# Kernel tuning notes

Hardware: AMD Instinct MI355X
Metric: run time of the kernel (lower is better)

## Reference

```python
import jax, jax.numpy as jnp
import numpy as np

HEAD_NUM = 16
SCALE = 1.0 / np.sqrt(HEAD_NUM)  # source divides by sqrt(head_num), not head_dim
MASK_VAL = -10000000.0


def setup_inputs() -> dict:
    key = jax.random.key(0)
    kq, kk, kv = jax.random.split(key, 3)
    shape = (2, 16, 2048, 64)  # [B, H, L, D]
    Q = jax.random.normal(kq, shape, dtype=jnp.float32)
    K = jax.random.normal(kk, shape, dtype=jnp.float32)
    V = jax.random.normal(kv, shape, dtype=jnp.float32)
    return {"Q": Q, "K": K, "V": V}


def reference(Q, K, V):
    L = Q.shape[-2]
    # [B, H, L, M] attention logits, scaled by 1/sqrt(head_num)
    logits = jnp.einsum('bhld,bhmd->bhlm', Q, K) * SCALE
    # causal mask: strictly-upper triangle gets -1e7 (additive, as in source)
    mask = jnp.triu(jnp.ones((L, L), dtype=logits.dtype), 1) * MASK_VAL
    logits = logits + mask[None, None, :, :]
    weights = jax.nn.softmax(logits, axis=-1)
    return jnp.einsum('bhlm,bhmd->bhld', weights, V)
```

## Files before the change

kernel.cpp:

```cpp
#include <hip/hip_runtime.h>
#include <hip/hip_bf16.h>

#define BM 128
#define BN 64
#define HD 64
#define LQ 2048
#define SD 72

typedef __attribute__((ext_vector_type(8))) short short8;
typedef __attribute__((ext_vector_type(16))) float f32x16;

#define QSCALE 0.360673760222241f

#define WS_HALF  ((size_t)32 * 2048 * 64)
#define WS_NEEDED (2 * WS_HALF * sizeof(unsigned short))

static __device__ __forceinline__ unsigned pk2(float a, float b) {
    union { __hip_bfloat162 h2; unsigned u; } c;
    c.h2 = __float22bfloat162_rn(make_float2(a, b));
    return c.u;
}

__global__ __launch_bounds__(256)
void prep(const float* __restrict__ Kg, const float* __restrict__ Vg,
          unsigned short* __restrict__ KF, unsigned short* __restrict__ VF) {
    __shared__ unsigned short sK2[64][72];
    __shared__ unsigned short sV2[64][72];
    const int t  = threadIdx.x;
    const int bx = blockIdx.x;
    const int bh = bx >> 5;
    const int c  = bx & 31;
    const size_t ibase = (size_t)bh * (LQ * HD) + (size_t)c * 64 * HD;
    const int r  = t >> 4;
    const int c4 = (t & 15) * 4;

#pragma unroll
    for (int p = 0; p < 4; ++p) {
        const int row = p * 16 + r;
        const float4 kv4 = *(const float4*)(Kg + ibase + (size_t)row * HD + c4);
        uint2 ku; ku.x = pk2(kv4.x, kv4.y); ku.y = pk2(kv4.z, kv4.w);
        *(uint2*)&sK2[row][c4] = ku;
        const float4 vv4 = *(const float4*)(Vg + ibase + (size_t)row * HD + c4);
        const unsigned u0 = pk2(vv4.x, vv4.y);
        const unsigned u1 = pk2(vv4.z, vv4.w);
        sV2[c4 + 0][row] = (unsigned short)(u0 & 0xffff);
        sV2[c4 + 1][row] = (unsigned short)(u0 >> 16);
        sV2[c4 + 2][row] = (unsigned short)(u1 & 0xffff);
        sV2[c4 + 3][row] = (unsigned short)(u1 >> 16);
    }
    __syncthreads();

    const int lane = t & 63;
    const int u    = t >> 6;
    const int l31  = lane & 31;
    const int hh   = lane >> 5;
#pragma unroll
    for (int e = 0; e < 2; ++e) {
        const int ch = 2 * c + e;
        const size_t ob = ((size_t)(bh * 64 + ch) * 4 + u) * 512 + lane * 8;
        *(uint4*)&KF[ob] = *(const uint4*)&sK2[e * 32 + l31][u * 16 + hh * 8];
        *(uint4*)&VF[ob] = *(const uint4*)&sV2[(u & 1) * 32 + l31][e * 32 + (u >> 1) * 16 + hh * 8];
    }
}

__global__ __launch_bounds__(256, 2)
void fa_main(const float* __restrict__ Qg,
             const unsigned short* __restrict__ KF,
             const unsigned short* __restrict__ VF,
             float* __restrict__ Og) {
    const int t    = threadIdx.x;
    const int w    = t >> 6;
    const int lane = t & 63;
    const int h    = lane >> 5;
    const int l31  = lane & 31;

    const int bx  = blockIdx.x;
    const int idx = (bx >> 5) & 7;
    const int qt  = (bx & 256) ? idx : (15 - idx);
    const int bh  = bx & 31;
    const int q0  = qt * BM;

    const size_t base = (size_t)bh * (LQ * HD);
    const unsigned short* KFh = KF + (size_t)bh * 131072 + lane * 8;
    const unsigned short* VFh = VF + (size_t)bh * 131072 + lane * 8;

    const int qrow = q0 + w * 32 + l31;
    short8 qreg[4];
    {
        const float* Qrow = Qg + base + (size_t)qrow * HD;
#pragma unroll
        for (int ks = 0; ks < 4; ++ks) {
            const float4 a = *(const float4*)(Qrow + ks * 16 + h * 8);
            const float4 b = *(const float4*)(Qrow + ks * 16 + h * 8 + 4);
            union { unsigned u[4]; short8 s8; } qu;
            qu.u[0] = pk2(a.x * QSCALE, a.y * QSCALE);
            qu.u[1] = pk2(a.z * QSCALE, a.w * QSCALE);
            qu.u[2] = pk2(b.x * QSCALE, b.y * QSCALE);
            qu.u[3] = pk2(b.z * QSCALE, b.w * QSCALE);
            qreg[ks] = qu.s8;
        }
    }

    f32x16 accO[2];
#pragma unroll
    for (int r = 0; r < 16; ++r) { accO[0][r] = 0.f; accO[1][r] = 0.f; }
    float lsum = 0.f;

    const int n_ch = (q0 >> 5) + w + 1;
    const int last = n_ch - 1;

    auto loadch = [&](short8* ak, short8* av, int ch) {
        const unsigned short* kp = KFh + (size_t)ch * 2048;
        ak[0] = *(const short8*)(kp);
        ak[1] = *(const short8*)(kp + 512);
        ak[2] = *(const short8*)(kp + 1024);
        ak[3] = *(const short8*)(kp + 1536);
        const unsigned short* vp = VFh + (size_t)ch * 2048;
        av[0] = *(const short8*)(vp);
        av[1] = *(const short8*)(vp + 512);
        av[2] = *(const short8*)(vp + 1024);
        av[3] = *(const short8*)(vp + 1536);
    };

    auto computech = [&](const short8* ak, const short8* av, int ch) {
        f32x16 accS;
#pragma unroll
        for (int r = 0; r < 16; ++r) accS[r] = 0.f;
        __builtin_amdgcn_s_setprio(1);
#pragma unroll
        for (int ks = 0; ks < 4; ++ks)
            accS = __builtin_amdgcn_mfma_f32_32x32x16_bf16(ak[ks], qreg[ks], accS, 0, 0, 0);
        __builtin_amdgcn_s_setprio(0);

        if (ch == last) {
            const int kvb = ch * 32 + 4 * h;
#pragma unroll
            for (int r = 0; r < 16; ++r) {
                const int kv = kvb + (r & 3) + 8 * (r >> 2);
                if (kv > qrow) accS[r] = -1e30f;
            }
        }

#pragma unroll
        for (int r = 0; r < 16; ++r) {
            const float p = __builtin_amdgcn_exp2f(accS[r]);
            accS[r] = p;
            lsum += p;
        }

        short8 pf[2];
#pragma unroll
        for (int s = 0; s < 2; ++s) {
            const int rb = s * 8;
            const unsigned a0 = pk2(accS[rb + 0], accS[rb + 1]);
            const unsigned b0 = pk2(accS[rb + 4], accS[rb + 5]);
            const unsigned a1 = pk2(accS[rb + 2], accS[rb + 3]);
            const unsigned b1 = pk2(accS[rb + 6], accS[rb + 7]);
            const auto r02 = __builtin_amdgcn_permlane32_swap(a0, b0, 0, 0);
            const auto r13 = __builtin_amdgcn_permlane32_swap(a1, b1, 0, 0);
            union { unsigned u[4]; short8 s8; } pu;
            pu.u[0] = r02[0]; pu.u[1] = r13[0]; pu.u[2] = r02[1]; pu.u[3] = r13[1];
            pf[s] = pu.s8;
        }

        __builtin_amdgcn_s_setprio(1);
#pragma unroll
        for (int s = 0; s < 2; ++s)
#pragma unroll
            for (int dg = 0; dg < 2; ++dg)
                accO[dg] = __builtin_amdgcn_mfma_f32_32x32x16_bf16(av[s * 2 + dg], pf[s], accO[dg], 0, 0, 0);
        __builtin_amdgcn_s_setprio(0);
    };

    short8 akA[4], avA[4], akB[4], avB[4];
    loadch(akA, avA, 0);
    int ch = 0;
    for (;;) {
        if (ch < last) loadch(akB, avB, ch + 1);
        computech(akA, avA, ch);
        if (++ch > last) break;
        if (ch < last) loadch(akA, avA, ch + 1);
        computech(akB, avB, ch);
        if (++ch > last) break;
    }

    lsum += __shfl_xor(lsum, 32);
    const float inv = 1.0f / lsum;
    float* Op = Og + base + (size_t)qrow * HD;
#pragma unroll
    for (int dg = 0; dg < 2; ++dg) {
#pragma unroll
        for (int rq = 0; rq < 4; ++rq) {
            const int d = dg * 32 + 8 * rq + 4 * h;
            float4 o;
            o.x = accO[dg][rq * 4 + 0] * inv;
            o.y = accO[dg][rq * 4 + 1] * inv;
            o.z = accO[dg][rq * 4 + 2] * inv;
            o.w = accO[dg][rq * 4 + 3] * inv;
            *(float4*)(Op + d) = o;
        }
    }
}

__global__ __launch_bounds__(512, 4)
void fa_fwd(const float* __restrict__ Qg,
            const float* __restrict__ Kg,
            const float* __restrict__ Vg,
            float* __restrict__ Og) {
    __shared__ __align__(16) unsigned short lds[(2 * BN + 2 * HD) * SD];
    typedef unsigned short KT[BN][SD];
    typedef unsigned short VT[HD][SD];
    KT* sK  = (KT*)lds;
    VT* sVt = (VT*)(lds + 2 * BN * SD);

    const int t    = threadIdx.x;
    const int w    = t >> 6;
    const int lane = t & 63;
    const int h    = lane >> 5;
    const int l31  = lane & 31;
    const int qd   = lane >> 4;
    const int qg   = w & 3;
    const int kh   = w >> 2;

    const int bx  = blockIdx.x;
    const int idx = (bx >> 5) & 7;
    const int qt  = (bx & 256) ? idx : (15 - idx);
    const int bh  = bx & 31;
    const int q0  = qt * BM;

    const size_t base = (size_t)bh * (LQ * HD);
    const float* Qp = Qg + base + (size_t)q0 * HD;
    const float* Kp = Kg + base;
    const float* Vp = Vg + base;

    const int r0 = t >> 4;
    const int c4 = (t & 15) * 4;
    const int RA = w * 4;

    {
        unsigned short (*sQ)[SD] = (unsigned short (*)[SD])lds;
#pragma unroll
        for (int p = 0; p < 4; ++p) {
            const int r = p * 32 + r0;
            const float4 v = *(const float4*)(Qp + (size_t)r * HD + c4);
            uint2 u;
            u.x = pk2(v.x * QSCALE, v.y * QSCALE);
            u.y = pk2(v.z * QSCALE, v.w * QSCALE);
            *(uint2*)&sQ[r][c4] = u;
        }
    }
    __syncthreads();
    short8 qreg[4];
    {
        unsigned short (*sQ)[SD] = (unsigned short (*)[SD])lds;
#pragma unroll
        for (int ks = 0; ks < 4; ++ks)
            qreg[ks] = *(const short8*)&sQ[qg * 32 + l31][ks * 16 + h * 8];
    }
    __syncthreads();

    float4 kA, kB, vA, vB;
    auto issue = [&](int kv0) {
        kA = *(const float4*)(Kp + (size_t)(kv0 + r0) * HD + c4);
        kB = *(const float4*)(Kp + (size_t)(kv0 + 32 + r0) * HD + c4);
        vA = *(const float4*)(Vp + (size_t)(kv0 + RA + qd) * HD + c4);
        vB = *(const float4*)(Vp + (size_t)(kv0 + 32 + RA + qd) * HD + c4);
    };
    auto vstore = [&](float4 vf, int R, int buf) {
        float e0 = vf.x, e1 = vf.y, e2 = vf.z, e3 = vf.w;
        float s0 = (qd & 2) ? e0 : e2;
        float s1 = (qd & 2) ? e1 : e3;
        s0 = __shfl_xor(s0, 32); s1 = __shfl_xor(s1, 32);
        if (qd & 2) { e0 = s0; e1 = s1; } else { e2 = s0; e3 = s1; }
        s0 = (qd & 1) ? e0 : e1;
        s1 = (qd & 1) ? e2 : e3;
        s0 = __shfl_xor(s0, 16); s1 = __shfl_xor(s1, 16);
        if (qd & 1) { e0 = s0; e2 = s1; } else { e1 = s0; e3 = s1; }
        const int d   = c4 + qd;
        const int col = ((((R >> 3) ^ (d >> 3)) & 7) << 3) | (R & 7);
        uint2 u; u.x = pk2(e0, e1); u.y = pk2(e2, e3);
        *(uint2*)&sVt[buf][d][col] = u;
    };
    auto commit = [&](int buf) {
        { uint2 u; u.x = pk2(kA.x, kA.y); u.y = pk2(kA.z, kA.w);
          *(uint2*)&sK[buf][r0][c4] = u; }
        { uint2 u; u.x = pk2(kB.x, kB.y); u.y = pk2(kB.z, kB.w);
          *(uint2*)&sK[buf][32 + r0][c4] = u; }
        vstore(vA, RA, buf);
        vstore(vB, 32 + RA, buf);
    };

    f32x16 accO[2];
#pragma unroll
    for (int r = 0; r < 16; ++r) { accO[0][r] = 0.f; accO[1][r] = 0.f; }
    float lsum = 0.f;

    const int qminw = q0 + qg * 32;
    const int qmaxw = qminw + 31;
    const int n_it  = (q0 + BM) / BN;

    issue(0);
    commit(0);

    for (int it = 0; it < n_it; ++it) {
        const int kv0 = it * BN;
        const int buf = it & 1;
        __syncthreads();
        const bool more = (it + 1 < n_it);
        if (more) issue(kv0 + BN);

        if (kv0 + kh * 32 <= qmaxw) {
            f32x16 accS;
#pragma unroll
            for (int r = 0; r < 16; ++r) accS[r] = 0.f;
            __builtin_amdgcn_s_setprio(1);
#pragma unroll
            for (int ks = 0; ks < 4; ++ks) {
                const short8 ak = *(const short8*)&sK[buf][kh * 32 + l31][ks * 16 + h * 8];
                accS = __builtin_amdgcn_mfma_f32_32x32x16_bf16(ak, qreg[ks], accS, 0, 0, 0);
            }
            __builtin_amdgcn_s_setprio(0);

            if (kv0 + kh * 32 + 31 > qminw) {
                const int qrow = qminw + l31;
                const int kvb  = kv0 + kh * 32 + 4 * h;
#pragma unroll
                for (int r = 0; r < 16; ++r) {
                    const int kv = kvb + (r & 3) + 8 * (r >> 2);
                    if (kv > qrow) accS[r] = -1e30f;
                }
            }
#pragma unroll
            for (int r = 0; r < 16; ++r) {
                const float p = __builtin_amdgcn_exp2f(accS[r]);
                accS[r] = p;
                lsum += p;
            }
            short8 pf[2];
#pragma unroll
            for (int s = 0; s < 2; ++s) {
                const int rb = s * 8;
                const unsigned a0 = pk2(accS[rb + 0], accS[rb + 1]);
                const unsigned b0 = pk2(accS[rb + 4], accS[rb + 5]);
                const unsigned a1 = pk2(accS[rb + 2], accS[rb + 3]);
                const unsigned b1 = pk2(accS[rb + 6], accS[rb + 7]);
                const auto r02 = __builtin_amdgcn_permlane32_swap(a0, b0, 0, 0);
                const auto r13 = __builtin_amdgcn_permlane32_swap(a1, b1, 0, 0);
                union { unsigned u[4]; short8 s8; } pu;
                pu.u[0] = r02[0]; pu.u[1] = r13[0]; pu.u[2] = r02[1]; pu.u[3] = r13[1];
                pf[s] = pu.s8;
            }
            __builtin_amdgcn_s_setprio(1);
#pragma unroll
            for (int s = 0; s < 2; ++s) {
                const int K0 = kh * 32 + s * 16 + h * 8;
#pragma unroll
                for (int dg = 0; dg < 2; ++dg) {
                    const int d   = dg * 32 + l31;
                    const int col = (((K0 >> 3) ^ (d >> 3)) & 7) << 3;
                    const short8 av = *(const short8*)&sVt[buf][d][col];
                    accO[dg] = __builtin_amdgcn_mfma_f32_32x32x16_bf16(av, pf[s], accO[dg], 0, 0, 0);
                }
            }
            __builtin_amdgcn_s_setprio(0);
        }

        if (more) commit(buf ^ 1);
    }

    lsum += __shfl_xor(lsum, 32);
    __syncthreads();
    float* fx  = (float*)lds;
    float* fla = fx + 4 * 64 * 32;
    if (kh == 1) {
#pragma unroll
        for (int dg = 0; dg < 2; ++dg) {
#pragma unroll
            for (int r = 0; r < 16; ++r) {
                const int d = dg * 32 + (r & 3) + 8 * (r >> 2) + 4 * h;
                fx[(qg * 64 + d) * 32 + l31] = accO[dg][r];
            }
        }
        if (h == 0) fla[qg * 32 + l31] = lsum;
    }
    __syncthreads();
    if (kh == 0) {
        const float inv  = 1.0f / (lsum + fla[qg * 32 + l31]);
        const int   qrow = q0 + qg * 32 + l31;
        float* Op = Og + base + (size_t)qrow * HD;
#pragma unroll
        for (int dg = 0; dg < 2; ++dg) {
#pragma unroll
            for (int rq = 0; rq < 4; ++rq) {
                const int d = dg * 32 + 8 * rq + 4 * h;
                const float* fr = &fx[(qg * 64 + d) * 32 + l31];
                float4 o;
                o.x = (accO[dg][rq * 4 + 0] + fr[0])  * inv;
                o.y = (accO[dg][rq * 4 + 1] + fr[32]) * inv;
                o.z = (accO[dg][rq * 4 + 2] + fr[64]) * inv;
                o.w = (accO[dg][rq * 4 + 3] + fr[96]) * inv;
                *(float4*)(Op + d) = o;
            }
        }
    }
}

extern "C" void kernel_launch(void* const* d_in, const int* in_sizes, int n_in,
                              void* d_out, int out_size, void* d_ws, size_t ws_size,
                              hipStream_t stream) {
    const float* Q = (const float*)d_in[0];
    const float* K = (const float*)d_in[1];
    const float* V = (const float*)d_in[2];
    float* O = (float*)d_out;
    if (d_ws != nullptr && ws_size >= WS_NEEDED) {
        unsigned short* KF = (unsigned short*)d_ws;
        unsigned short* VF = KF + WS_HALF;
        prep<<<dim3(1024), dim3(256), 0, stream>>>(K, V, KF, VF);
        fa_main<<<dim3(512), dim3(256), 0, stream>>>(Q, KF, VF, O);
    } else {
        fa_fwd<<<dim3(512), dim3(512), 0, stream>>>(Q, K, V, O);
    }
}
```

Baseline: 125.0 us.

## Split KV chunks across two wave groups per query tile and reduce via LDS

fa_main now launches 512 threads per block, where two groups of four waves share each query slice and process alternating (even/odd) 32-wide KV chunks. Partial output accumulators and row sums from the odd group go through shared memory, and the even group combines them and writes the result. K is prefetched two chunks ahead while V is loaded just in time inside the compute step, which cuts register use. The aim is to double wave-level parallelism and halve the serial chunk loop per wave, at the cost of an LDS reduction, a block barrier, and higher occupancy demands.

Measured after the change: 119.0 us. 1.05x faster.

```diff
diff --git a/kernel.cpp b/kernel.cpp
--- a/kernel.cpp
+++ b/kernel.cpp
@@ -63,16 +63,21 @@
     }
 }
 
-__global__ __launch_bounds__(256, 2)
+__global__ __launch_bounds__(512, 4)
 void fa_main(const float* __restrict__ Qg,
              const unsigned short* __restrict__ KF,
              const unsigned short* __restrict__ VF,
              float* __restrict__ Og) {
+    __shared__ float fx[4 * 64 * 32];
+    __shared__ float fla[4 * 32];
+
     const int t    = threadIdx.x;
     const int w    = t >> 6;
     const int lane = t & 63;
     const int h    = lane >> 5;
     const int l31  = lane & 31;
+    const int qg   = w & 3;
+    const int kp   = w >> 2;
 
     const int bx  = blockIdx.x;
     const int idx = (bx >> 5) & 7;
@@ -84,7 +89,9 @@
     const unsigned short* KFh = KF + (size_t)bh * 131072 + lane * 8;
     const unsigned short* VFh = VF + (size_t)bh * 131072 + lane * 8;
 
-    const int qrow = q0 + w * 32 + l31;
+    const int j    = 4 * qt + qg;
+    const int qrow = j * 32 + l31;
+
     short8 qreg[4];
     {
         const float* Qrow = Qg + base + (size_t)qrow * HD;
@@ -106,23 +113,24 @@
     for (int r = 0; r < 16; ++r) { accO[0][r] = 0.f; accO[1][r] = 0.f; }
     float lsum = 0.f;
 
-    const int n_ch = (q0 >> 5) + w + 1;
-    const int last = n_ch - 1;
-
-    auto loadch = [&](short8* ak, short8* av, int ch) {
-        const unsigned short* kp = KFh + (size_t)ch * 2048;
-        ak[0] = *(const short8*)(kp);
-        ak[1] = *(const short8*)(kp + 512);
-        ak[2] = *(const short8*)(kp + 1024);
-        ak[3] = *(const short8*)(kp + 1536);
+    auto loadK = [&](short8* ak, int ch) {
+        const unsigned short* kpt = KFh + (size_t)ch * 2048;
+        ak[0] = *(const short8*)(kpt);
+        ak[1] = *(const short8*)(kpt + 512);
+        ak[2] = *(const short8*)(kpt + 1024);
+        ak[3] = *(const short8*)(kpt + 1536);
+    };
+
+    auto computech = [&](const short8* ak, short8* akNext, int ch, bool pre) {
+        short8 av[4];
         const unsigned short* vp = VFh + (size_t)ch * 2048;
         av[0] = *(const short8*)(vp);
         av[1] = *(const short8*)(vp + 512);
         av[2] = *(const short8*)(vp + 1024);
         av[3] = *(const short8*)(vp + 1536);
-    };
-
-    auto computech = [&](const short8* ak, const short8* av, int ch) {
+        if (pre) loadK(akNext, ch + 2);
+        __builtin_amdgcn_sched_barrier(0);
+
         f32x16 accS;
 #pragma unroll
         for (int r = 0; r < 16; ++r) accS[r] = 0.f;
@@ -132,7 +140,7 @@
             accS = __builtin_amdgcn_mfma_f32_32x32x16_bf16(ak[ks], qreg[ks], accS, 0, 0, 0);
         __builtin_amdgcn_s_setprio(0);
 
-        if (ch == last) {
+        if (ch == j) {
             const int kvb = ch * 32 + 4 * h;
 #pragma unroll
             for (int r = 0; r < 16; ++r) {
@@ -172,32 +180,49 @@
         __builtin_amdgcn_s_setprio(0);
     };
 
-    short8 akA[4], avA[4], akB[4], avB[4];
-    loadch(akA, avA, 0);
-    int ch = 0;
-    for (;;) {
-        if (ch < last) loadch(akB, avB, ch + 1);
-        computech(akA, avA, ch);
-        if (++ch > last) break;
-        if (ch < last) loadch(akA, avA, ch + 1);
-        computech(akB, avB, ch);
-        if (++ch > last) break;
+    short8 akA[4], akB[4];
+    int ch = kp;
+    if (ch <= j) {
+        loadK(akA, ch);
+        for (;;) {
+            computech(akA, akB, ch, ch + 2 <= j);
+            ch += 2;
+            if (ch > j) break;
+            computech(akB, akA, ch, ch + 2 <= j);
+            ch += 2;
+            if (ch > j) break;
+        }
     }
 
     lsum += __shfl_xor(lsum, 32);
-    const float inv = 1.0f / lsum;
-    float* Op = Og + base + (size_t)qrow * HD;
-#pragma unroll
-    for (int dg = 0; dg < 2; ++dg) {
-#pragma unroll
-        for (int rq = 0; rq < 4; ++rq) {
-            const int d = dg * 32 + 8 * rq + 4 * h;
-            float4 o;
-            o.x = accO[dg][rq * 4 + 0] * inv;
-            o.y = accO[dg][rq * 4 + 1] * inv;
-            o.z = accO[dg][rq * 4 + 2] * inv;
-            o.w = accO[dg][rq * 4 + 3] * inv;
-            *(float4*)(Op + d) = o;
+    if (kp == 1) {
+#pragma unroll
+        for (int dg = 0; dg < 2; ++dg) {
+#pragma unroll
+            for (int r = 0; r < 16; ++r) {
+                const int d = dg * 32 + (r & 3) + 8 * (r >> 2) + 4 * h;
+                fx[(qg * 64 + d) * 32 + l31] = accO[dg][r];
+            }
+        }
+        if (h == 0) fla[qg * 32 + l31] = lsum;
+    }
+    __syncthreads();
+    if (kp == 0) {
+        const float inv = 1.0f / (lsum + fla[qg * 32 + l31]);
+        float* Op = Og + base + (size_t)qrow * HD;
+#pragma unroll
+        for (int dg = 0; dg < 2; ++dg) {
+#pragma unroll
+            for (int rq = 0; rq < 4; ++rq) {
+                const int d = dg * 32 + 8 * rq + 4 * h;
+                const float* fr = &fx[(qg * 64 + d) * 32 + l31];
+                float4 o;
+                o.x = (accO[dg][rq * 4 + 0] + fr[0])  * inv;
+                o.y = (accO[dg][rq * 4 + 1] + fr[32]) * inv;
+                o.z = (accO[dg][rq * 4 + 2] + fr[64]) * inv;
+                o.w = (accO[dg][rq * 4 + 3] + fr[96]) * inv;
+                *(float4*)(Op + d) = o;
+            }
         }
     }
 }
@@ -416,7 +441,7 @@
         unsigned short* KF = (unsigned short*)d_ws;
         unsigned short* VF = KF + WS_HALF;
         prep<<<dim3(1024), dim3(256), 0, stream>>>(K, V, KF, VF);
-        fa_main<<<dim3(512), dim3(256), 0, stream>>>(Q, KF, VF, O);
+        fa_main<<<dim3(512), dim3(512), 0, stream>>>(Q, KF, VF, O);
     } else {
         fa_fwd<<<dim3(512), dim3(512), 0, stream>>>(Q, K, V, O);
     }
```
